# Kernel optimization log

Hardware: AMD Instinct MI355X
Metric: run time of the kernel (lower is better)

The kernel has to match this reference:

```python
import jax, jax.numpy as jnp
import numpy as np

N_NODES = 100000
N_EDGES = 1600000
N_GRAPHS = 512


def gcn_conv(x, src, dst, W, b, num_nodes):
    """PyG GCNConv: add self-loops, sym-normalize, aggregate, add bias."""
    xw = x @ W  # [N, out]
    # degree over destination nodes, +1 for the implicit self-loop
    deg = jax.ops.segment_sum(jnp.ones(src.shape[0], xw.dtype), dst,
                              num_segments=num_nodes) + 1.0
    dinv = jax.lax.rsqrt(deg)  # deg >= 1, safe
    norm = dinv[src] * dinv[dst]  # [E]
    agg = jax.ops.segment_sum(xw[src] * norm[:, None], dst,
                              num_segments=num_nodes)
    # self-loop contribution: dinv[i]^2 * xw[i]
    agg = agg + xw * (dinv * dinv)[:, None]
    return agg + b


def global_mean_pool(x, batch, num_graphs):
    sums = jax.ops.segment_sum(x, batch, num_segments=num_graphs)
    cnts = jax.ops.segment_sum(jnp.ones(x.shape[0], x.dtype), batch,
                               num_segments=num_graphs)
    return sums / jnp.maximum(cnts, 1.0)[:, None]


def setup_inputs() -> dict:
    key = jax.random.key(0)
    ks = jax.random.split(key, 9)
    x = jax.random.normal(ks[0], (N_NODES, 3), dtype=jnp.float32)
    edge_index = jax.random.randint(ks[1], (2, N_EDGES), 0, N_NODES, dtype=jnp.int64)
    batch = jnp.sort(jax.random.randint(ks[2], (N_NODES,), 0, N_GRAPHS, dtype=jnp.int64))
    W1 = jax.random.normal(ks[3], (3, 32), dtype=jnp.float32) * 0.5
    b1 = jax.random.normal(ks[4], (32,), dtype=jnp.float32) * 0.1
    W2 = jax.random.normal(ks[5], (32, 32), dtype=jnp.float32) * 0.2
    b2 = jax.random.normal(ks[6], (32,), dtype=jnp.float32) * 0.1
    Wl = jax.random.normal(ks[7], (32, 2), dtype=jnp.float32) * 0.2
    bl = jax.random.normal(ks[8], (2,), dtype=jnp.float32) * 0.1
    return {"x": x, "edge_index": edge_index, "batch": batch,
            "W1": W1, "b1": b1, "W2": W2, "b2": b2, "Wl": Wl, "bl": bl}


def reference(x, edge_index, batch, W1, b1, W2, b2, Wl, bl):
    src, dst = edge_index[0], edge_index[1]
    h = jax.nn.relu(gcn_conv(x, src, dst, W1, b1, N_NODES))
    h = jax.nn.relu(gcn_conv(h, src, dst, W2, b2, N_NODES))
    g = global_mean_pool(h, batch, N_GRAPHS)  # [G, 32]
    return g @ Wl + bl  # [G, 2]
```

## Files before the change

kernel.cpp:

```cpp
#include <hip/hip_runtime.h>
#include <hip/hip_fp16.h>

#define NN 100000
#define NE 1600000
#define NG 512
#define F  32

#define BSH    8
#define BNODES 256
#define NB     ((NN + BNODES - 1) / BNODES)
#define CAP    5120
#define PCHUNK 4096
#define NWGP   ((NE + PCHUNK - 1) / PCHUNK)

__global__ void k_partition(const int* __restrict__ src, const int* __restrict__ dst,
                            int* __restrict__ cursor, int* __restrict__ part) {
    __shared__ int hist[NB];
    __shared__ int base[NB];
    int tid = threadIdx.x;
    for (int i = tid; i < NB; i += 512) hist[i] = 0;
    __syncthreads();
    int e0 = blockIdx.x * PCHUNK;
    int e1 = min(e0 + PCHUNK, NE);
    for (int e = e0 + tid; e < e1; e += 512) atomicAdd(&hist[dst[e] >> BSH], 1);
    __syncthreads();
    for (int i = tid; i < NB; i += 512) {
        base[i] = hist[i] ? (i * CAP + atomicAdd(&cursor[i], hist[i])) : 0;
        hist[i] = 0;
    }
    __syncthreads();
    for (int e = e0 + tid; e < e1; e += 512) {
        int d = dst[e];
        int b = d >> BSH;
        int p = base[b] + atomicAdd(&hist[b], 1);
        part[p] = (src[e] << 8) | (d & (BNODES - 1));
    }
}

__global__ void k_fill2(const int* __restrict__ part, const int* __restrict__ cursor,
                        const float* __restrict__ x,
                        int* __restrict__ rowpack, float* __restrict__ dinv,
                        float4* __restrict__ xd, int* __restrict__ csr) {
    __shared__ int cnt[BNODES];
    __shared__ int off[BNODES];
    __shared__ int lds[BNODES];
    int b = blockIdx.x, tid = threadIdx.x;
    int node0 = b << BSH;
    int s0 = b * CAP;
    int s1 = s0 + cursor[b];
    cnt[tid] = 0;
    __syncthreads();
    for (int i = s0 + tid; i < s1; i += 256) atomicAdd(&cnt[part[i] & (BNODES - 1)], 1);
    __syncthreads();
    int c = cnt[tid];
    lds[tid] = c;
    __syncthreads();
    for (int o = 1; o < 256; o <<= 1) {
        int t = (tid >= o) ? lds[tid - o] : 0;
        __syncthreads();
        lds[tid] += t;
        __syncthreads();
    }
    int excl = lds[tid] - c;
    off[tid] = excl;
    int n = node0 + tid;
    if (n < NN) {
        rowpack[n] = ((s0 + excl) << 10) | c;
        float d = rsqrtf((float)c + 1.0f);
        dinv[n] = d;
        xd[n] = make_float4(d * x[n * 3 + 0], d * x[n * 3 + 1], d * x[n * 3 + 2], d);
    }
    __syncthreads();
    for (int i = s0 + tid; i < s1; i += 256) {
        int p = part[i];
        int pos = s0 + atomicAdd(&off[p & (BNODES - 1)], 1);
        csr[pos] = p >> 8;
    }
}

__global__ void k_agg1p(const int* __restrict__ rowpack, const int* __restrict__ csr,
                        const float4* __restrict__ xd,
                        const float* __restrict__ W1, const float* __restrict__ b1,
                        __half2* __restrict__ g1) {
    __shared__ float W1s[3 * F];
    __shared__ float b1s[F];
    int tid = threadIdx.x;
    if (tid < 3 * F) W1s[tid] = W1[tid];
    if (tid < F) b1s[tid] = b1[tid];
    __syncthreads();
    int n = blockIdx.x * blockDim.x + tid;
    if (n >= NN) return;
    int pack = rowpack[n];
    int beg = pack >> 10, end = beg + (pack & 1023);
    float ax = 0.0f, ay = 0.0f, az = 0.0f;
    int e = beg;
    for (; e + 3 < end; e += 4) {
        int s0 = csr[e], s1 = csr[e + 1], s2 = csr[e + 2], s3 = csr[e + 3];
        float4 v0 = xd[s0], v1 = xd[s1], v2 = xd[s2], v3 = xd[s3];
        ax += (v0.x + v1.x) + (v2.x + v3.x);
        ay += (v0.y + v1.y) + (v2.y + v3.y);
        az += (v0.z + v1.z) + (v2.z + v3.z);
    }
    for (; e < end; ++e) {
        float4 v = xd[csr[e]];
        ax += v.x; ay += v.y; az += v.z;
    }
    float4 sf = xd[n];
    float dn = sf.w;
    float cx = dn * (ax + sf.x), cy = dn * (ay + sf.y), cz = dn * (az + sf.z);
    __half2 tmp[16];
#pragma unroll
    for (int j = 0; j < 16; ++j) {
        int f0 = 2 * j, f1 = 2 * j + 1;
        float v0 = cx * W1s[f0] + cy * W1s[F + f0] + cz * W1s[2 * F + f0] + b1s[f0];
        float v1 = cx * W1s[f1] + cy * W1s[F + f1] + cz * W1s[2 * F + f1] + b1s[f1];
        tmp[j] = __floats2half2_rn(dn * fmaxf(v0, 0.0f), dn * fmaxf(v1, 0.0f));
    }
    uint4* hv = (uint4*)(g1 + (size_t)n * 16);
    const uint4* tv = (const uint4*)tmp;
    hv[0] = tv[0]; hv[1] = tv[1]; hv[2] = tv[2]; hv[3] = tv[3];
}

__global__ void k_gather2h(const int* __restrict__ rowpack, const int* __restrict__ csr,
                           const __half2* __restrict__ g1, const float* __restrict__ dinv,
                           __half2* __restrict__ t16) {
    int tid = threadIdx.x;
    int n = blockIdx.x * 16 + (tid >> 4);
    if (n >= NN) return;
    int j = tid & 15;
    int pack = rowpack[n];
    int beg = pack >> 10, end = beg + (pack & 1023);
    float ax = 0.0f, ay = 0.0f;
    int e = beg;
    for (; e + 3 < end; e += 4) {
        int s0 = csr[e], s1 = csr[e + 1], s2 = csr[e + 2], s3 = csr[e + 3];
        float2 v0 = __half22float2(g1[s0 * 16 + j]);
        float2 v1 = __half22float2(g1[s1 * 16 + j]);
        float2 v2 = __half22float2(g1[s2 * 16 + j]);
        float2 v3 = __half22float2(g1[s3 * 16 + j]);
        ax += (v0.x + v1.x) + (v2.x + v3.x);
        ay += (v0.y + v1.y) + (v2.y + v3.y);
    }
    for (; e < end; ++e) {
        float2 v = __half22float2(g1[csr[e] * 16 + j]);
        ax += v.x;
        ay += v.y;
    }
    float dn = dinv[n];
    float2 sf = __half22float2(g1[n * 16 + j]);
    t16[n * 16 + j] = __floats2half2_rn(dn * (ax + sf.x), dn * (ay + sf.y));
}

__global__ void k_proj2_pool_head(const __half2* __restrict__ t16,
                                  const int* __restrict__ batch,
                                  const float* __restrict__ W2, const float* __restrict__ b2,
                                  const float* __restrict__ Wl, const float* __restrict__ bl,
                                  float* __restrict__ out) {
    __shared__ float W2s[F * F];
    __shared__ float ts[8][F];
    __shared__ float red[8][F];
    __shared__ float mean[F];
    __shared__ int range[2];
    int g = blockIdx.x, tid = threadIdx.x;
    for (int i = tid; i < F * F; i += 256) W2s[i] = W2[i];
    if (tid < 2) {
        int key = g + tid, lo = 0, hi = NN;
        while (lo < hi) {
            int mid = (lo + hi) >> 1;
            if (batch[mid] < key) lo = mid + 1; else hi = mid;
        }
        range[tid] = lo;
    }
    __syncthreads();
    int s = range[0], e = range[1];
    int grp = tid >> 5, f = tid & 31;
    float b2f = b2[f];
    float psum = 0.0f;
    for (int n0 = s; n0 < e; n0 += 8) {
        __syncthreads();
        if (tid < 128) {
            int nl = tid >> 4, j = tid & 15;
            int n = n0 + nl;
            if (n < e) {
                float2 v = __half22float2(t16[n * 16 + j]);
                ts[nl][2 * j]     = v.x;
                ts[nl][2 * j + 1] = v.y;
            }
        }
        __syncthreads();
        int n = n0 + grp;
        if (n < e) {
            float acc = b2f;
#pragma unroll
            for (int k = 0; k < F; k++) acc += ts[grp][k] * W2s[k * F + f];
            psum += fmaxf(acc, 0.0f);
        }
    }
    red[grp][f] = psum;
    __syncthreads();
    if (grp == 0) {
        float t = red[0][f] + red[1][f] + red[2][f] + red[3][f]
                + red[4][f] + red[5][f] + red[6][f] + red[7][f];
        mean[f] = t / fmaxf((float)(e - s), 1.0f);
    }
    __syncthreads();
    if (tid < 2) {
        float a = 0.0f;
#pragma unroll
        for (int k = 0; k < F; k++) a += mean[k] * Wl[k * 2 + tid];
        out[g * 2 + tid] = a + bl[tid];
    }
}

extern "C" void kernel_launch(void* const* d_in, const int* in_sizes, int n_in,
                              void* d_out, int out_size, void* d_ws, size_t ws_size,
                              hipStream_t stream) {
    const float* x     = (const float*)d_in[0];
    const int*   eidx  = (const int*)d_in[1];
    const int*   batch = (const int*)d_in[2];
    const float* W1    = (const float*)d_in[3];
    const float* b1    = (const float*)d_in[4];
    const float* W2    = (const float*)d_in[5];
    const float* b2    = (const float*)d_in[6];
    const float* Wl    = (const float*)d_in[7];
    const float* bl    = (const float*)d_in[8];
    float*       out   = (float*)d_out;

    const int* src = eidx;
    const int* dst = eidx + NE;

    char* base = (char*)d_ws;
    size_t off = 0;
    auto alloc = [&](size_t bytes) {
        void* p = base + off;
        off = (off + bytes + 127) & ~(size_t)127;
        return p;
    };
    int*     cursor  = (int*)alloc(NB * sizeof(int));
    int*     rowpack = (int*)alloc(NN * sizeof(int));
    int*     part    = (int*)alloc((size_t)NB * CAP * sizeof(int));
    int*     csr     = (int*)alloc((size_t)NB * CAP * sizeof(int));
    float*   dinv    = (float*)alloc(NN * sizeof(float));
    float4*  xd      = (float4*)alloc(NN * sizeof(float4));
    __half2* g1      = (__half2*)alloc((size_t)NN * 16 * sizeof(__half2));
    __half2* t16     = (__half2*)alloc((size_t)NN * 16 * sizeof(__half2));

    const int B = 256;
    const int gN   = (NN + B - 1) / B;
    const int gG16 = (NN + 15) / 16;

    hipMemsetAsync(cursor, 0, NB * sizeof(int), stream);
    k_partition<<<NWGP, 512, 0, stream>>>(src, dst, cursor, part);
    k_fill2    <<<NB,   B,   0, stream>>>(part, cursor, x, rowpack, dinv, xd, csr);

    k_agg1p<<<gN, B, 0, stream>>>(rowpack, csr, xd, W1, b1, g1);

    k_gather2h<<<gG16, B, 0, stream>>>(rowpack, csr, g1, dinv, t16);

    k_proj2_pool_head<<<NG, B, 0, stream>>>(t16, batch, W2, b2, Wl, bl, out);
}
```

Measured before the change: 188.4 us.

## Fuse CSR scatter with layer-1 aggregation and layer-2 gather with projection and pooling

The fill kernel is split in two. The second half builds each bucket's CSR slice in LDS and immediately runs the layer-1 gather from LDS indices, computing the layer-1 output in the same kernel. The layer-2 gather now also applies W2, ReLU and a per-graph partial sum via atomics into a small gsum buffer, so the t16 intermediate and the per-graph pooling kernel go away. A small head kernel finishes the mean and the final linear layer. The cost is an extra launch, float atomics whose order can vary between runs, and a grid of NN/16 that relies on NN being divisible by 16.

```diff
diff --git a/kernel.cpp b/kernel.cpp
--- a/kernel.cpp
+++ b/kernel.cpp
@@ -37,17 +37,15 @@
     }
 }
 
-__global__ void k_fill2(const int* __restrict__ part, const int* __restrict__ cursor,
-                        const float* __restrict__ x,
-                        int* __restrict__ rowpack, float* __restrict__ dinv,
-                        float4* __restrict__ xd, int* __restrict__ csr) {
+__global__ void k_fill2a(const int* __restrict__ part, const int* __restrict__ cursor,
+                         const float* __restrict__ x,
+                         int* __restrict__ rowpack, float* __restrict__ dinv,
+                         float4* __restrict__ xd) {
     __shared__ int cnt[BNODES];
-    __shared__ int off[BNODES];
     __shared__ int lds[BNODES];
     int b = blockIdx.x, tid = threadIdx.x;
     int node0 = b << BSH;
-    int s0 = b * CAP;
-    int s1 = s0 + cursor[b];
+    int s0 = b * CAP, s1 = s0 + cursor[b];
     cnt[tid] = 0;
     __syncthreads();
     for (int i = s0 + tid; i < s1; i += 256) atomicAdd(&cnt[part[i] & (BNODES - 1)], 1);
@@ -62,7 +60,6 @@
         __syncthreads();
     }
     int excl = lds[tid] - c;
-    off[tid] = excl;
     int n = node0 + tid;
     if (n < NN) {
         rowpack[n] = ((s0 + excl) << 10) | c;
@@ -70,146 +67,152 @@
         dinv[n] = d;
         xd[n] = make_float4(d * x[n * 3 + 0], d * x[n * 3 + 1], d * x[n * 3 + 2], d);
     }
-    __syncthreads();
-    for (int i = s0 + tid; i < s1; i += 256) {
-        int p = part[i];
-        int pos = s0 + atomicAdd(&off[p & (BNODES - 1)], 1);
-        csr[pos] = p >> 8;
-    }
-}
-
-__global__ void k_agg1p(const int* __restrict__ rowpack, const int* __restrict__ csr,
-                        const float4* __restrict__ xd,
-                        const float* __restrict__ W1, const float* __restrict__ b1,
-                        __half2* __restrict__ g1) {
+}
+
+__global__ void k_fill2b(const int* __restrict__ part, const int* __restrict__ cursor,
+                         const int* __restrict__ rowpack, const float4* __restrict__ xd,
+                         const float* __restrict__ W1, const float* __restrict__ b1,
+                         int* __restrict__ csr, __half2* __restrict__ g1) {
+    __shared__ int lcsr[CAP];
+    __shared__ int off[BNODES];
     __shared__ float W1s[3 * F];
     __shared__ float b1s[F];
-    int tid = threadIdx.x;
+    int b = blockIdx.x, tid = threadIdx.x;
+    int node0 = b << BSH;
+    int s0 = b * CAP;
+    int cnt = cursor[b];
     if (tid < 3 * F) W1s[tid] = W1[tid];
     if (tid < F) b1s[tid] = b1[tid];
-    __syncthreads();
-    int n = blockIdx.x * blockDim.x + tid;
-    if (n >= NN) return;
-    int pack = rowpack[n];
-    int beg = pack >> 10, end = beg + (pack & 1023);
-    float ax = 0.0f, ay = 0.0f, az = 0.0f;
-    int e = beg;
-    for (; e + 3 < end; e += 4) {
-        int s0 = csr[e], s1 = csr[e + 1], s2 = csr[e + 2], s3 = csr[e + 3];
-        float4 v0 = xd[s0], v1 = xd[s1], v2 = xd[s2], v3 = xd[s3];
-        ax += (v0.x + v1.x) + (v2.x + v3.x);
-        ay += (v0.y + v1.y) + (v2.y + v3.y);
-        az += (v0.z + v1.z) + (v2.z + v3.z);
-    }
-    for (; e < end; ++e) {
-        float4 v = xd[csr[e]];
-        ax += v.x; ay += v.y; az += v.z;
-    }
-    float4 sf = xd[n];
-    float dn = sf.w;
-    float cx = dn * (ax + sf.x), cy = dn * (ay + sf.y), cz = dn * (az + sf.z);
-    __half2 tmp[16];
-#pragma unroll
-    for (int j = 0; j < 16; ++j) {
-        int f0 = 2 * j, f1 = 2 * j + 1;
-        float v0 = cx * W1s[f0] + cy * W1s[F + f0] + cz * W1s[2 * F + f0] + b1s[f0];
-        float v1 = cx * W1s[f1] + cy * W1s[F + f1] + cz * W1s[2 * F + f1] + b1s[f1];
-        tmp[j] = __floats2half2_rn(dn * fmaxf(v0, 0.0f), dn * fmaxf(v1, 0.0f));
-    }
-    uint4* hv = (uint4*)(g1 + (size_t)n * 16);
-    const uint4* tv = (const uint4*)tmp;
-    hv[0] = tv[0]; hv[1] = tv[1]; hv[2] = tv[2]; hv[3] = tv[3];
-}
-
-__global__ void k_gather2h(const int* __restrict__ rowpack, const int* __restrict__ csr,
+    int n = node0 + tid;
+    int pack = (n < NN) ? rowpack[n] : (s0 << 10);
+    off[tid] = (pack >> 10) - s0;
+    __syncthreads();
+    for (int i = tid; i < cnt; i += 256) {
+        int p = part[s0 + i];
+        int pos = atomicAdd(&off[p & (BNODES - 1)], 1);
+        lcsr[pos] = p >> 8;
+    }
+    __syncthreads();
+    for (int i = tid; i < cnt; i += 256) csr[s0 + i] = lcsr[i];
+    if (n < NN) {
+        int deg = pack & 1023;
+        int beg = (pack >> 10) - s0;
+        int end = beg + deg;
+        float ax = 0.0f, ay = 0.0f, az = 0.0f;
+        int e = beg;
+        for (; e + 3 < end; e += 4) {
+            int i0 = lcsr[e], i1 = lcsr[e + 1], i2 = lcsr[e + 2], i3 = lcsr[e + 3];
+            float4 v0 = xd[i0], v1 = xd[i1], v2 = xd[i2], v3 = xd[i3];
+            ax += (v0.x + v1.x) + (v2.x + v3.x);
+            ay += (v0.y + v1.y) + (v2.y + v3.y);
+            az += (v0.z + v1.z) + (v2.z + v3.z);
+        }
+        for (; e < end; ++e) {
+            float4 v = xd[lcsr[e]];
+            ax += v.x; ay += v.y; az += v.z;
+        }
+        float4 sf = xd[n];
+        float dn = sf.w;
+        float cx = dn * (ax + sf.x), cy = dn * (ay + sf.y), cz = dn * (az + sf.z);
+        __half2 tmp[16];
+#pragma unroll
+        for (int j = 0; j < 16; ++j) {
+            int f0 = 2 * j, f1 = 2 * j + 1;
+            float v0 = cx * W1s[f0] + cy * W1s[F + f0] + cz * W1s[2 * F + f0] + b1s[f0];
+            float v1 = cx * W1s[f1] + cy * W1s[F + f1] + cz * W1s[2 * F + f1] + b1s[f1];
+            tmp[j] = __floats2half2_rn(dn * fmaxf(v0, 0.0f), dn * fmaxf(v1, 0.0f));
+        }
+        uint4* hv = (uint4*)(g1 + (size_t)n * 16);
+        const uint4* tv = (const uint4*)tmp;
+        hv[0] = tv[0]; hv[1] = tv[1]; hv[2] = tv[2]; hv[3] = tv[3];
+    }
+}
+
+__global__ void k_gather2p(const int* __restrict__ rowpack, const int* __restrict__ csr,
                            const __half2* __restrict__ g1, const float* __restrict__ dinv,
-                           __half2* __restrict__ t16) {
+                           const int* __restrict__ batch,
+                           const float* __restrict__ W2, const float* __restrict__ b2,
+                           float* __restrict__ gsum) {
+    __shared__ float W2s[F * F];
+    __shared__ float b2s[F];
+    __shared__ float ts[16][F];
+    __shared__ float hs[16][F];
+    __shared__ int bat[16];
     int tid = threadIdx.x;
-    int n = blockIdx.x * 16 + (tid >> 4);
-    if (n >= NN) return;
-    int j = tid & 15;
-    int pack = rowpack[n];
-    int beg = pack >> 10, end = beg + (pack & 1023);
-    float ax = 0.0f, ay = 0.0f;
-    int e = beg;
-    for (; e + 3 < end; e += 4) {
-        int s0 = csr[e], s1 = csr[e + 1], s2 = csr[e + 2], s3 = csr[e + 3];
-        float2 v0 = __half22float2(g1[s0 * 16 + j]);
-        float2 v1 = __half22float2(g1[s1 * 16 + j]);
-        float2 v2 = __half22float2(g1[s2 * 16 + j]);
-        float2 v3 = __half22float2(g1[s3 * 16 + j]);
-        ax += (v0.x + v1.x) + (v2.x + v3.x);
-        ay += (v0.y + v1.y) + (v2.y + v3.y);
-    }
-    for (; e < end; ++e) {
-        float2 v = __half22float2(g1[csr[e] * 16 + j]);
-        ax += v.x;
-        ay += v.y;
-    }
-    float dn = dinv[n];
-    float2 sf = __half22float2(g1[n * 16 + j]);
-    t16[n * 16 + j] = __floats2half2_rn(dn * (ax + sf.x), dn * (ay + sf.y));
-}
-
-__global__ void k_proj2_pool_head(const __half2* __restrict__ t16,
-                                  const int* __restrict__ batch,
-                                  const float* __restrict__ W2, const float* __restrict__ b2,
-                                  const float* __restrict__ Wl, const float* __restrict__ bl,
-                                  float* __restrict__ out) {
-    __shared__ float W2s[F * F];
-    __shared__ float ts[8][F];
-    __shared__ float red[8][F];
-    __shared__ float mean[F];
-    __shared__ int range[2];
-    int g = blockIdx.x, tid = threadIdx.x;
+    int nb = blockIdx.x * 16;
     for (int i = tid; i < F * F; i += 256) W2s[i] = W2[i];
-    if (tid < 2) {
-        int key = g + tid, lo = 0, hi = NN;
-        while (lo < hi) {
-            int mid = (lo + hi) >> 1;
-            if (batch[mid] < key) lo = mid + 1; else hi = mid;
-        }
-        range[tid] = lo;
-    }
-    __syncthreads();
-    int s = range[0], e = range[1];
-    int grp = tid >> 5, f = tid & 31;
-    float b2f = b2[f];
-    float psum = 0.0f;
-    for (int n0 = s; n0 < e; n0 += 8) {
-        __syncthreads();
-        if (tid < 128) {
-            int nl = tid >> 4, j = tid & 15;
-            int n = n0 + nl;
-            if (n < e) {
-                float2 v = __half22float2(t16[n * 16 + j]);
-                ts[nl][2 * j]     = v.x;
-                ts[nl][2 * j + 1] = v.y;
-            }
-        }
-        __syncthreads();
-        int n = n0 + grp;
-        if (n < e) {
-            float acc = b2f;
-#pragma unroll
-            for (int k = 0; k < F; k++) acc += ts[grp][k] * W2s[k * F + f];
-            psum += fmaxf(acc, 0.0f);
-        }
-    }
-    red[grp][f] = psum;
-    __syncthreads();
-    if (grp == 0) {
-        float t = red[0][f] + red[1][f] + red[2][f] + red[3][f]
-                + red[4][f] + red[5][f] + red[6][f] + red[7][f];
-        mean[f] = t / fmaxf((float)(e - s), 1.0f);
-    }
-    __syncthreads();
-    if (tid < 2) {
-        float a = 0.0f;
-#pragma unroll
-        for (int k = 0; k < F; k++) a += mean[k] * Wl[k * 2 + tid];
-        out[g * 2 + tid] = a + bl[tid];
-    }
+    if (tid < F) b2s[tid] = b2[tid];
+    if (tid < 16) bat[tid] = batch[nb + tid];
+    int nl = tid >> 4, j = tid & 15;
+    int n = nb + nl;
+    {
+        int pack = rowpack[n];
+        int beg = pack >> 10, end = beg + (pack & 1023);
+        float ax = 0.0f, ay = 0.0f;
+        int e = beg;
+        for (; e + 3 < end; e += 4) {
+            int s0 = csr[e], s1 = csr[e + 1], s2 = csr[e + 2], s3 = csr[e + 3];
+            float2 v0 = __half22float2(g1[s0 * 16 + j]);
+            float2 v1 = __half22float2(g1[s1 * 16 + j]);
+            float2 v2 = __half22float2(g1[s2 * 16 + j]);
+            float2 v3 = __half22float2(g1[s3 * 16 + j]);
+            ax += (v0.x + v1.x) + (v2.x + v3.x);
+            ay += (v0.y + v1.y) + (v2.y + v3.y);
+        }
+        for (; e < end; ++e) {
+            float2 v = __half22float2(g1[csr[e] * 16 + j]);
+            ax += v.x; ay += v.y;
+        }
+        float dn = dinv[n];
+        float2 sf = __half22float2(g1[n * 16 + j]);
+        ts[nl][2 * j]     = dn * (ax + sf.x);
+        ts[nl][2 * j + 1] = dn * (ay + sf.y);
+    }
+    __syncthreads();
+    {
+        int f = tid & 31;
+        int nn0 = tid >> 5;
+#pragma unroll
+        for (int pass = 0; pass < 2; ++pass) {
+            int nn = nn0 + pass * 8;
+            float acc = b2s[f];
+#pragma unroll
+            for (int k = 0; k < F; ++k) acc += ts[nn][k] * W2s[k * F + f];
+            hs[nn][f] = fmaxf(acc, 0.0f);
+        }
+    }
+    __syncthreads();
+    if (tid < F) {
+        int g0 = bat[0], gmax = bat[15];
+        for (int g = g0; g <= gmax; ++g) {
+            float s = 0.0f;
+#pragma unroll
+            for (int i = 0; i < 16; ++i) if (bat[i] == g) s += hs[i][tid];
+            atomicAdd(&gsum[g * F + tid], s);
+        }
+    }
+}
+
+__global__ void k_head(const float* __restrict__ gsum, const int* __restrict__ batch,
+                       const float* __restrict__ Wl, const float* __restrict__ bl,
+                       float* __restrict__ out) {
+    int g = blockIdx.x * blockDim.x + threadIdx.x;
+    if (g >= NG) return;
+    int lo = 0, hi = NN;
+    while (lo < hi) { int m = (lo + hi) >> 1; if (batch[m] < g) lo = m + 1; else hi = m; }
+    int s = lo;
+    lo = 0; hi = NN;
+    while (lo < hi) { int m = (lo + hi) >> 1; if (batch[m] < g + 1) lo = m + 1; else hi = m; }
+    float inv = 1.0f / fmaxf((float)(lo - s), 1.0f);
+    float a0 = 0.0f, a1 = 0.0f;
+#pragma unroll
+    for (int k = 0; k < F; ++k) {
+        float m = gsum[g * F + k] * inv;
+        a0 += m * Wl[k * 2 + 0];
+        a1 += m * Wl[k * 2 + 1];
+    }
+    out[g * 2 + 0] = a0 + bl[0];
+    out[g * 2 + 1] = a1 + bl[1];
 }
 
 extern "C" void kernel_launch(void* const* d_in, const int* in_sizes, int n_in,
@@ -243,19 +246,19 @@
     float*   dinv    = (float*)alloc(NN * sizeof(float));
     float4*  xd      = (float4*)alloc(NN * sizeof(float4));
     __half2* g1      = (__half2*)alloc((size_t)NN * 16 * sizeof(__half2));
-    __half2* t16     = (__half2*)alloc((size_t)NN * 16 * sizeof(__half2));
+    float*   gsum    = (float*)alloc((size_t)NG * F * sizeof(float));
 
     const int B = 256;
-    const int gN   = (NN + B - 1) / B;
-    const int gG16 = (NN + 15) / 16;
+    const int gG16 = NN / 16;
 
     hipMemsetAsync(cursor, 0, NB * sizeof(int), stream);
+    hipMemsetAsync(gsum, 0, (size_t)NG * F * sizeof(float), stream);
+
     k_partition<<<NWGP, 512, 0, stream>>>(src, dst, cursor, part);
-    k_fill2    <<<NB,   B,   0, stream>>>(part, cursor, x, rowpack, dinv, xd, csr);
-
-    k_agg1p<<<gN, B, 0, stream>>>(rowpack, csr, xd, W1, b1, g1);
-
-    k_gather2h<<<gG16, B, 0, stream>>>(rowpack, csr, g1, dinv, t16);
-
-    k_proj2_pool_head<<<NG, B, 0, stream>>>(t16, batch, W2, b2, Wl, bl, out);
-}
+    k_fill2a   <<<NB,   B,   0, stream>>>(part, cursor, x, rowpack, dinv, xd);
+    k_fill2b   <<<NB,   B,   0, stream>>>(part, cursor, rowpack, xd, W1, b1, csr, g1);
+
+    k_gather2p<<<gG16, B, 0, stream>>>(rowpack, csr, g1, dinv, batch, W2, b2, gsum);
+
+    k_head<<<(NG + B - 1) / B, B, 0, stream>>>(gsum, batch, Wl, bl, out);
+}
```

Result: faster. 177.3 us (-5.9%).
